# Performance work log

Hardware: AMD Instinct MI355X
Metric: run time of the kernel (lower is better)

The kernel has to match this reference:

```python
import jax, jax.numpy as jnp
import numpy as np

N_NODES = 100000
N_EDGES = 3200000
HID = 16
MP_ROUNDS = 3


def _mlp(w1, b1, w2, b2, x):
    # channels-first MLP applied per edge/node: x is [C_in, E]
    h = jax.nn.relu(w1 @ x + b1[:, None])
    return w2 @ h + b2[:, None]


def setup_inputs() -> dict:
    key = jax.random.key(0)
    ks = jax.random.split(key, 20)
    s = lambda k, shp: jax.random.normal(k, shp, dtype=jnp.float32) * 0.1
    inp = {
        "nodes": jax.random.normal(ks[0], (N_NODES,), dtype=jnp.float32),
        "edges_init": jax.random.normal(ks[1], (N_EDGES,), dtype=jnp.float32),
        "senders": jax.random.randint(ks[2], (N_EDGES,), 0, N_NODES, dtype=jnp.int32),
        "receivers": jax.random.randint(ks[3], (N_EDGES,), 0, N_NODES, dtype=jnp.int32),
        # EdgeEncoder: 1 -> HID -> HID
        "enc_w1": s(ks[4], (HID, 1)), "enc_b1": jnp.zeros((HID,), jnp.float32),
        "enc_w2": s(ks[5], (HID, HID)), "enc_b2": jnp.zeros((HID,), jnp.float32),
        # Node update MLP: (1 + 2*HID) -> HID -> 1  (shared across rounds)
        "node_w1": s(ks[6], (HID, 1 + 2 * HID)), "node_b1": jnp.zeros((HID,), jnp.float32),
        "node_w2": s(ks[7], (1, HID)), "node_b2": jnp.zeros((1,), jnp.float32),
        # Edge update MLP: (HID + 2) -> HID -> HID  (shared across rounds)
        "edge_w1": s(ks[8], (HID, HID + 2)), "edge_b1": jnp.zeros((HID,), jnp.float32),
        "edge_w2": s(ks[9], (HID, HID)), "edge_b2": jnp.zeros((HID,), jnp.float32),
        # EdgeDecoder: HID -> HID -> 1
        "dec_w1": s(ks[10], (HID, HID)), "dec_b1": jnp.zeros((HID,), jnp.float32),
        "dec_w2": s(ks[11], (1, HID)), "dec_b2": jnp.zeros((1,), jnp.float32),
        "alpha": jnp.float32(0.1),
    }
    return inp


def reference(nodes, edges_init, senders, receivers,
              enc_w1, enc_b1, enc_w2, enc_b2,
              node_w1, node_b1, node_w2, node_b2,
              edge_w1, edge_b1, edge_w2, edge_b2,
              dec_w1, dec_b1, dec_w2, dec_b2, alpha):
    n_nodes = nodes.shape[0]
    norm = jnp.abs(edges_init).max()
    e = edges_init / norm                      # [E]
    e = _mlp(enc_w1, enc_b1, enc_w2, enc_b2, e[None, :])   # [HID, E]
    for _ in range(MP_ROUNDS):                 # shared-weight MP blocks
        # gather/scatter: aggregate edge features to nodes
        agg_s = jax.ops.segment_sum(e.T, senders, num_segments=n_nodes).T     # [HID, N]
        agg_r = jax.ops.segment_sum(e.T, receivers, num_segments=n_nodes).T   # [HID, N]
        node_in = jnp.concatenate([nodes[None, :], agg_s, agg_r], axis=0)     # [1+2H, N]
        nodes = _mlp(node_w1, node_b1, node_w2, node_b2, node_in)[0]          # [N]
        edge_in = jnp.concatenate([e, nodes[senders][None, :], nodes[receivers][None, :]], axis=0)  # [H+2, E]
        e = _mlp(edge_w1, edge_b1, edge_w2, edge_b2, edge_in)                 # [HID, E]
    e = _mlp(dec_w1, dec_b1, dec_w2, dec_b2, e)[0]          # [E]
    low_tri_data = edges_init + alpha * (e * norm)          # L = L + alpha*GNN(L)
    return low_tri_data
```

## Files before the change

kernel.cpp:

```cpp
#include <hip/hip_runtime.h>
#include <hip/hip_bf16.h>

#define N_NODES 100000
#define N_EDGES 3200000
#define HID 16
#define NB 256
#define NPB 391
#define SCAP 15360
#define RCAP 15360
#define FDEPTH 32
#define LCAP1 8704
#define LCAP2 26624

static constexpr int BLK = 256;

__device__ __forceinline__ float frelu(float x) { return fmaxf(x, 0.f); }
__device__ __forceinline__ float bflo(unsigned int u) {
  return __uint_as_float(u << 16);
}
__device__ __forceinline__ float bfhi(unsigned int u) {
  return __uint_as_float(u & 0xFFFF0000u);
}
__device__ __forceinline__ unsigned int packbf(float lo, float hi) {
  __hip_bfloat16 hl = __float2bfloat16(lo), hh = __float2bfloat16(hi);
  return ((unsigned int)(*(unsigned short*)&hh) << 16) |
         (unsigned int)(*(unsigned short*)&hl);
}

union E16 {
  float4 f4[2];
  __hip_bfloat16 h[16];
};

__global__ __launch_bounds__(256) void k_norm(const float* __restrict__ edges,
                                              unsigned int* __restrict__ normbits) {
  float m = 0.f;
  for (int i = blockIdx.x * blockDim.x + threadIdx.x; i < N_EDGES;
       i += gridDim.x * blockDim.x)
    m = fmaxf(m, fabsf(edges[i]));
#pragma unroll
  for (int off = 32; off > 0; off >>= 1)
    m = fmaxf(m, __shfl_down(m, off, 64));
  __shared__ float smax[BLK / 64];
  if ((threadIdx.x & 63) == 0) smax[threadIdx.x >> 6] = m;
  __syncthreads();
  if (threadIdx.x == 0) {
    float b = smax[0];
#pragma unroll
    for (int w = 1; w < BLK / 64; ++w) b = fmaxf(b, smax[w]);
    atomicMax(normbits, __float_as_uint(b));
  }
}

__global__ __launch_bounds__(1024) void k_split(
    const int* __restrict__ senders, const int* __restrict__ receivers,
    const float* __restrict__ edges, int* __restrict__ gcnt,
    unsigned int* __restrict__ pM, float* __restrict__ pV,
    unsigned int* __restrict__ pO) {
  __shared__ __align__(16) unsigned int fM[NB][FDEPTH];
  __shared__ __align__(16) unsigned int fV[NB][FDEPTH];
  __shared__ __align__(16) unsigned int fO[NB][FDEPTH];
  __shared__ int fcnt[NB];
  const int t = threadIdx.x;
  if (t < NB) fcnt[t] = 0;
  __syncthreads();
  const int e0 = blockIdx.x * (N_EDGES / 256);
  const int e1 = e0 + (N_EDGES / 256);
  for (int base = e0; base < e1; base += 1024) {
    const int i = base + t;
    if (i < e1) {
      int s = senders[i];
      unsigned int b = (unsigned int)s / NPB;
      unsigned int m = (((unsigned int)s - b * NPB) << 22) | (unsigned int)i;
      unsigned int v = __float_as_uint(edges[i]);
      unsigned int o = (unsigned int)receivers[i];
      int pos = atomicAdd(&fcnt[b], 1);
      if (pos < FDEPTH) {
        fM[b][pos] = m; fV[b][pos] = v; fO[b][pos] = o;
      } else {
        int gb = atomicAdd(&gcnt[b], 1);
        if (gb < SCAP) {
          pM[(size_t)b * SCAP + gb] = m;
          pV[(size_t)b * SCAP + gb] = __uint_as_float(v);
          pO[(size_t)b * SCAP + gb] = o;
        }
      }
    }
    __syncthreads();
    const bool last = (base + 1024 >= e1);
    if (t < NB) {
      int c = fcnt[t]; if (c > FDEPTH) c = FDEPTH;
      int nf = last ? c : (c & ~15);
      if (nf > 0) {
        int gb = atomicAdd(&gcnt[t], nf);
        size_t db = (size_t)t * SCAP + gb;
        if ((gb & 3) == 0 && gb + nf <= SCAP) {
          int k = 0;
          for (; k + 4 <= nf; k += 4) {
            *(uint4*)(pM + db + k) = *(const uint4*)(&fM[t][k]);
            *(uint4*)((unsigned int*)pV + db + k) = *(const uint4*)(&fV[t][k]);
            *(uint4*)(pO + db + k) = *(const uint4*)(&fO[t][k]);
          }
          for (; k < nf; ++k) {
            pM[db + k] = fM[t][k]; pV[db + k] = __uint_as_float(fV[t][k]);
            pO[db + k] = fO[t][k];
          }
        } else {
          for (int k = 0; k < nf; ++k)
            if (gb + k < SCAP) {
              pM[db + k] = fM[t][k]; pV[db + k] = __uint_as_float(fV[t][k]);
              pO[db + k] = fO[t][k];
            }
        }
        int res = c - nf;
        for (int k = 0; k < res; ++k) {
          fM[t][k] = fM[t][nf + k]; fV[t][k] = fV[t][nf + k];
          fO[t][k] = fO[t][nf + k];
        }
        fcnt[t] = res;
      } else fcnt[t] = c;
    }
    __syncthreads();
  }
}

__global__ __launch_bounds__(1024) void k_bsort1(
    const unsigned int* __restrict__ pM, const float* __restrict__ pV,
    const unsigned int* __restrict__ pO, const int* __restrict__ gcnt,
    unsigned int* __restrict__ srecv, unsigned int* __restrict__ sorig,
    unsigned short* __restrict__ svalbf, unsigned int* __restrict__ ssend32,
    int* __restrict__ soff) {
  __shared__ unsigned int sM[LCAP1];
  __shared__ float sV[LCAP1];
  __shared__ unsigned int sO[LCAP1];
  __shared__ int hist[NPB], pref[NPB + 1], sc[NPB], cur[NPB];
  __shared__ int bb[NB];
  __shared__ int base_s;
  const int b = blockIdx.x, t = threadIdx.x, nt = blockDim.x;
  if (t < NB) { int c = gcnt[t]; bb[t] = c > SCAP ? SCAP : c; }
  for (int k = t; k < NPB; k += nt) hist[k] = 0;
  __syncthreads();
  if (t == 0) { int s = 0; for (int k = 0; k < b; ++k) s += bb[k]; base_s = s; }
  int nb = gcnt[b]; if (nb > SCAP) nb = SCAP;
  const unsigned int* PM = pM + (size_t)b * SCAP;
  const float* PV = pV + (size_t)b * SCAP;
  const unsigned int* PO = pO + (size_t)b * SCAP;
  for (int i = t; i < nb; i += nt) atomicAdd(&hist[PM[i] >> 22], 1);
  __syncthreads();
  if (t < NPB) sc[t] = hist[t];
  __syncthreads();
  for (int d = 1; d < NPB; d <<= 1) {
    int add = 0;
    if (t < NPB && t >= d) add = sc[t - d];
    __syncthreads();
    if (t < NPB && t >= d) sc[t] += add;
    __syncthreads();
  }
  if (t < NPB) pref[t] = sc[t] - hist[t];
  if (t == 0) pref[NPB] = sc[NPB - 1];
  __syncthreads();
  const int base = base_s;
  const int node0 = b * NPB;
  for (int k = t; k < NPB; k += nt) {
    int n = node0 + k;
    if (n < N_NODES) soff[n] = base + pref[k];
  }
  if (b == NB - 1 && t == 0) soff[N_NODES] = base + nb;
  __syncthreads();
  int klo = 0;
  while (klo < NPB) {
    int base0 = pref[klo];
    int khi = klo;
    while (khi < NPB && pref[khi + 1] - base0 <= LCAP1) ++khi;
    if (khi == klo) khi = klo + 1;
    for (int k = klo + t; k < khi; k += nt) cur[k] = pref[k];
    __syncthreads();
    for (int i = t; i < nb; i += nt) {
      unsigned int m = PM[i];
      int key = (int)(m >> 22);
      if (key >= klo && key < khi) {
        int p = atomicAdd(&cur[key], 1) - base0;
        if (p < LCAP1) { sM[p] = m; sV[p] = PV[i]; sO[p] = PO[i]; }
      }
    }
    __syncthreads();
    int csz = pref[khi] - base0;
    for (int i = t; i < csz; i += nt) {
      int g = base + base0 + i;
      unsigned int m = sM[i];
      srecv[g] = sO[i]; sorig[g] = m & 0x3FFFFFu;
      ssend32[g] = (unsigned int)(node0 + (int)(m >> 22));
      __hip_bfloat16 hb = __float2bfloat16(sV[i]);
      svalbf[g] = *(unsigned short*)&hb;
    }
    __syncthreads();
    klo = khi;
  }
}

__global__ __launch_bounds__(1024) void k_rsplit(
    const unsigned int* __restrict__ srecv, int* __restrict__ gcnt2,
    unsigned int* __restrict__ rpA) {
  __shared__ __align__(16) unsigned int fA[NB][FDEPTH];
  __shared__ int fcnt[NB];
  const int t = threadIdx.x;
  if (t < NB) fcnt[t] = 0;
  __syncthreads();
  const int e0 = blockIdx.x * (N_EDGES / 256);
  const int e1 = e0 + (N_EDGES / 256);
  for (int base = e0; base < e1; base += 1024) {
    const int i = base + t;
    if (i < e1) {
      unsigned int r = srecv[i];
      unsigned int b = r / NPB;
      unsigned int a = ((r - b * NPB) << 22) | (unsigned int)i;
      int pos = atomicAdd(&fcnt[b], 1);
      if (pos < FDEPTH) {
        fA[b][pos] = a;
      } else {
        int gb = atomicAdd(&gcnt2[b], 1);
        if (gb < RCAP) rpA[(size_t)b * RCAP + gb] = a;
      }
    }
    __syncthreads();
    const bool last = (base + 1024 >= e1);
    if (t < NB) {
      int c = fcnt[t]; if (c > FDEPTH) c = FDEPTH;
      int nf = last ? c : (c & ~15);
      if (nf > 0) {
        int gb = atomicAdd(&gcnt2[t], nf);
        size_t db = (size_t)t * RCAP + gb;
        if ((gb & 3) == 0 && gb + nf <= RCAP) {
          int k = 0;
          for (; k + 4 <= nf; k += 4)
            *(uint4*)(rpA + db + k) = *(const uint4*)(&fA[t][k]);
          for (; k < nf; ++k) rpA[db + k] = fA[t][k];
        } else {
          for (int k = 0; k < nf; ++k)
            if (gb + k < RCAP) rpA[db + k] = fA[t][k];
        }
        int res = c - nf;
        for (int k = 0; k < res; ++k) fA[t][k] = fA[t][nf + k];
        fcnt[t] = res;
      } else fcnt[t] = c;
    }
    __syncthreads();
  }
}

__global__ __launch_bounds__(1024) void k_rsort(
    const unsigned int* __restrict__ rpA, const int* __restrict__ gcnt2,
    unsigned int* __restrict__ rlist, int* __restrict__ roff) {
  __shared__ unsigned int sA[LCAP2];
  __shared__ int hist[NPB], pref[NPB + 1], sc[NPB], cur[NPB];
  __shared__ int bb[NB];
  __shared__ int base_s;
  const int b = blockIdx.x, t = threadIdx.x, nt = blockDim.x;
  if (t < NB) { int c = gcnt2[t]; bb[t] = c > RCAP ? RCAP : c; }
  for (int k = t; k < NPB; k += nt) hist[k] = 0;
  __syncthreads();
  if (t == 0) { int s = 0; for (int k = 0; k < b; ++k) s += bb[k]; base_s = s; }
  int nb = gcnt2[b]; if (nb > RCAP) nb = RCAP;
  const unsigned int* PA = rpA + (size_t)b * RCAP;
  for (int i = t; i < nb; i += nt) atomicAdd(&hist[PA[i] >> 22], 1);
  __syncthreads();
  if (t < NPB) sc[t] = hist[t];
  __syncthreads();
  for (int d = 1; d < NPB; d <<= 1) {
    int add = 0;
    if (t < NPB && t >= d) add = sc[t - d];
    __syncthreads();
    if (t < NPB && t >= d) sc[t] += add;
    __syncthreads();
  }
  if (t < NPB) pref[t] = sc[t] - hist[t];
  if (t == 0) pref[NPB] = sc[NPB - 1];
  __syncthreads();
  const int base = base_s;
  const int node0 = b * NPB;
  for (int k = t; k < NPB; k += nt) {
    int n = node0 + k;
    if (n < N_NODES) roff[n] = base + pref[k];
  }
  if (b == NB - 1 && t == 0) roff[N_NODES] = base + nb;
  __syncthreads();
  int klo = 0;
  while (klo < NPB) {
    int base0 = pref[klo];
    int khi = klo;
    while (khi < NPB && pref[khi + 1] - base0 <= LCAP2) ++khi;
    if (khi == klo) khi = klo + 1;
    for (int k = klo + t; k < khi; k += nt) cur[k] = pref[k];
    __syncthreads();
    for (int i = t; i < nb; i += nt) {
      unsigned int a = PA[i];
      int key = (int)(a >> 22);
      if (key >= klo && key < khi) {
        int p = atomicAdd(&cur[key], 1) - base0;
        if (p < LCAP2) sA[p] = a;
      }
    }
    __syncthreads();
    int csz = pref[khi] - base0;
    for (int i = t; i < csz; i += nt)
      rlist[base + base0 + i] = sA[i] & 0x3FFFFFu;
    __syncthreads();
    klo = khi;
  }
}

__global__ __launch_bounds__(256) void k_encode(
    const unsigned short* __restrict__ svalbf, const float* __restrict__ w1,
    const float* __restrict__ b1, const float* __restrict__ w2,
    const float* __restrict__ b2, const unsigned int* __restrict__ normbits,
    unsigned short* __restrict__ e) {
  int i = blockIdx.x * blockDim.x + threadIdx.x;
  float norm = __uint_as_float(*normbits);
  float x = bflo((unsigned int)svalbf[i]) / norm;
  float h[HID];
#pragma unroll
  for (int j = 0; j < HID; ++j) h[j] = frelu(fmaf(w1[j], x, b1[j]));
  E16 o;
#pragma unroll
  for (int j = 0; j < HID; ++j) {
    float acc = b2[j];
#pragma unroll
    for (int k = 0; k < HID; ++k) acc = fmaf(w2[j * HID + k], h[k], acc);
    o.h[j] = __float2bfloat16(acc);
  }
  float4* ep = (float4*)(e + (size_t)i * HID);
  ep[0] = o.f4[0];
  ep[1] = o.f4[1];
}

__global__ __launch_bounds__(256) void k_aggN(
    const unsigned short* __restrict__ e, const int* __restrict__ roff,
    const unsigned int* __restrict__ rlist, const int* __restrict__ soff,
    const float* __restrict__ nodesr, const float* __restrict__ nw1,
    const float* __restrict__ nb1_, const float* __restrict__ nw2,
    const float* __restrict__ nb2_, float* __restrict__ nodesw) {
  int wave = (blockIdx.x * blockDim.x + threadIdx.x) >> 6;
  int lane = threadIdx.x & 63, half = lane >> 5, l32 = lane & 31;
  int n = wave * 2 + half;
  int sub = l32 & 1, j16 = l32 >> 1;
  int r0 = roff[n], rdeg = roff[n + 1] - r0;
  float ar[8] = {0, 0, 0, 0, 0, 0, 0, 0};
  int q0 = 0;
  int full2 = rdeg & ~31;
  for (; q0 < full2; q0 += 32) {
    int idx0 = r0 + q0 + j16;
    unsigned int si0 = rlist[idx0];
    unsigned int si1 = rlist[idx0 + 16];
    uint4 ra = *(const uint4*)(e + (size_t)si0 * HID + sub * 8);
    uint4 rb = *(const uint4*)(e + (size_t)si1 * HID + sub * 8);
    ar[0] += bflo(ra.x); ar[1] += bfhi(ra.x);
    ar[2] += bflo(ra.y); ar[3] += bfhi(ra.y);
    ar[4] += bflo(ra.z); ar[5] += bfhi(ra.z);
    ar[6] += bflo(ra.w); ar[7] += bfhi(ra.w);
    ar[0] += bflo(rb.x); ar[1] += bfhi(rb.x);
    ar[2] += bflo(rb.y); ar[3] += bfhi(rb.y);
    ar[4] += bflo(rb.z); ar[5] += bfhi(rb.z);
    ar[6] += bflo(rb.w); ar[7] += bfhi(rb.w);
  }
  if (q0 + 16 <= rdeg) {
    int idx = r0 + q0 + j16;
    unsigned int si = rlist[idx];
    uint4 raw = *(const uint4*)(e + (size_t)si * HID + sub * 8);
    ar[0] += bflo(raw.x); ar[1] += bfhi(raw.x);
    ar[2] += bflo(raw.y); ar[3] += bfhi(raw.y);
    ar[4] += bflo(raw.z); ar[5] += bfhi(raw.z);
    ar[6] += bflo(raw.w); ar[7] += bfhi(raw.w);
    q0 += 16;
  }
  if (q0 < rdeg) {
    int slot = q0 + j16;
    bool ok = slot < rdeg;
    int idx = r0 + (ok ? slot : 0);
    unsigned int si = rlist[idx];
    uint4 raw = *(const uint4*)(e + (size_t)si * HID + sub * 8);
    float okf = ok ? 1.f : 0.f;
    ar[0] = fmaf(bflo(raw.x), okf, ar[0]); ar[1] = fmaf(bfhi(raw.x), okf, ar[1]);
    ar[2] = fmaf(bflo(raw.y), okf, ar[2]); ar[3] = fmaf(bfhi(raw.y), okf, ar[3]);
    ar[4] = fmaf(bflo(raw.z), okf, ar[4]); ar[5] = fmaf(bfhi(raw.z), okf, ar[5]);
    ar[6] = fmaf(bflo(raw.w), okf, ar[6]); ar[7] = fmaf(bfhi(raw.w), okf, ar[7]);
  }
#pragma unroll
  for (int off = 16; off >= 2; off >>= 1)
#pragma unroll
    for (int c = 0; c < 8; ++c) ar[c] += __shfl_down(ar[c], off, 64);
  int s0 = soff[n], sdeg = soff[n + 1] - s0;
  float as[16];
#pragma unroll
  for (int c = 0; c < 16; ++c) as[c] = 0.f;
  int fullB = sdeg & ~31;
  int c0 = 0;
  for (; c0 < fullB; c0 += 32) {
    int idx = s0 + c0 + l32;
    uint4 ra = *(const uint4*)(e + (size_t)idx * HID);
    uint4 rb = *(const uint4*)(e + (size_t)idx * HID + 8);
    as[0] += bflo(ra.x);  as[1] += bfhi(ra.x);
    as[2] += bflo(ra.y);  as[3] += bfhi(ra.y);
    as[4] += bflo(ra.z);  as[5] += bfhi(ra.z);
    as[6] += bflo(ra.w);  as[7] += bfhi(ra.w);
    as[8] += bflo(rb.x);  as[9] += bfhi(rb.x);
    as[10] += bflo(rb.y); as[11] += bfhi(rb.y);
    as[12] += bflo(rb.z); as[13] += bfhi(rb.z);
    as[14] += bflo(rb.w); as[15] += bfhi(rb.w);
  }
  if (c0 < sdeg) {
    int k = c0 + l32;
    bool ok = k < sdeg;
    int idx = s0 + (ok ? k : 0);
    uint4 ra = *(const uint4*)(e + (size_t)idx * HID);
    uint4 rb = *(const uint4*)(e + (size_t)idx * HID + 8);
    float okf = ok ? 1.f : 0.f;
    as[0] = fmaf(bflo(ra.x), okf, as[0]);  as[1] = fmaf(bfhi(ra.x), okf, as[1]);
    as[2] = fmaf(bflo(ra.y), okf, as[2]);  as[3] = fmaf(bfhi(ra.y), okf, as[3]);
    as[4] = fmaf(bflo(ra.z), okf, as[4]);  as[5] = fmaf(bfhi(ra.z), okf, as[5]);
    as[6] = fmaf(bflo(ra.w), okf, as[6]);  as[7] = fmaf(bfhi(ra.w), okf, as[7]);
    as[8] = fmaf(bflo(rb.x), okf, as[8]);  as[9] = fmaf(bfhi(rb.x), okf, as[9]);
    as[10] = fmaf(bflo(rb.y), okf, as[10]); as[11] = fmaf(bfhi(rb.y), okf, as[11]);
    as[12] = fmaf(bflo(rb.z), okf, as[12]); as[13] = fmaf(bfhi(rb.z), okf, as[13]);
    as[14] = fmaf(bflo(rb.w), okf, as[14]); as[15] = fmaf(bfhi(rb.w), okf, as[15]);
  }
#pragma unroll
  for (int off = 16; off >= 1; off >>= 1)
#pragma unroll
    for (int c = 0; c < 16; ++c) as[c] += __shfl_down(as[c], off, 64);
  float aS[16], aR[16];
#pragma unroll
  for (int c = 0; c < 16; ++c) aS[c] = __shfl(as[c], half * 32, 64);
#pragma unroll
  for (int k = 0; k < 8; ++k) aR[k] = __shfl(ar[k], half * 32, 64);
#pragma unroll
  for (int k = 0; k < 8; ++k) aR[8 + k] = __shfl(ar[k], half * 32 + 1, 64);
  float nsv = nodesr[n];
  float pv = 0.f;
  if (l32 < 16) {
    int j = l32;
    float a1 = fmaf(nw1[j * 33], nsv, nb1_[j]);
#pragma unroll
    for (int k = 0; k < 16; ++k) a1 = fmaf(nw1[j * 33 + 1 + k], aS[k], a1);
#pragma unroll
    for (int k = 0; k < 16; ++k) a1 = fmaf(nw1[j * 33 + 17 + k], aR[k], a1);
    pv = nw2[j] * frelu(a1);
  }
#pragma unroll
  for (int off = 8; off >= 1; off >>= 1) pv += __shfl_down(pv, off, 64);
  if (l32 == 0) nodesw[n] = pv + nb2_[0];
}

__global__ __launch_bounds__(256, 4) void k_edgeE(
    unsigned short* __restrict__ e, const unsigned int* __restrict__ srecv,
    const unsigned int* __restrict__ ssend32, const float* __restrict__ nodes,
    const float* __restrict__ w1, const float* __restrict__ b1,
    const float* __restrict__ w2, const float* __restrict__ b2) {
  int i0 = (blockIdx.x * blockDim.x + threadIdx.x) * 2;
  float ns[2], nr[2];
#pragma unroll
  for (int q = 0; q < 2; ++q) {
    ns[q] = nodes[ssend32[i0 + q]];
    nr[q] = nodes[srecv[i0 + q]];
  }
  unsigned int pk[2][8];
#pragma unroll
  for (int q = 0; q < 2; ++q) {
    const uint4* ep = (const uint4*)(e + (size_t)(i0 + q) * HID);
    uint4 ra = ep[0], rb = ep[1];
    pk[q][0] = ra.x; pk[q][1] = ra.y; pk[q][2] = ra.z; pk[q][3] = ra.w;
    pk[q][4] = rb.x; pk[q][5] = rb.y; pk[q][6] = rb.z; pk[q][7] = rb.w;
  }
  float h[2][16];
#pragma unroll
  for (int j = 0; j < 16; ++j) {
    float wA = w1[j * 18 + 16], wB = w1[j * 18 + 17], bb = b1[j];
#pragma unroll
    for (int q = 0; q < 2; ++q)
      h[q][j] = fmaf(wA, ns[q], fmaf(wB, nr[q], bb));
  }
#pragma unroll
  for (int kp = 0; kp < 8; ++kp) {
    float x0[2], x1[2];
#pragma unroll
    for (int q = 0; q < 2; ++q) {
      x0[q] = bflo(pk[q][kp]);
      x1[q] = bfhi(pk[q][kp]);
    }
#pragma unroll
    for (int j = 0; j < 16; ++j) {
      float wA = w1[j * 18 + 2 * kp], wB = w1[j * 18 + 2 * kp + 1];
#pragma unroll
      for (int q = 0; q < 2; ++q)
        h[q][j] = fmaf(wB, x1[q], fmaf(wA, x0[q], h[q][j]));
    }
  }
#pragma unroll
  for (int j = 0; j < 16; ++j)
#pragma unroll
    for (int q = 0; q < 2; ++q) h[q][j] = frelu(h[q][j]);
#pragma unroll
  for (int c0 = 0; c0 < 16; c0 += 8) {
    float y[2][8];
#pragma unroll
    for (int cc = 0; cc < 8; ++cc) {
      float bv = b2[c0 + cc];
#pragma unroll
      for (int q = 0; q < 2; ++q) y[q][cc] = bv;
    }
#pragma unroll
    for (int j = 0; j < 16; ++j) {
#pragma unroll
      for (int cc = 0; cc < 8; ++cc) {
        float wv = w2[(c0 + cc) * HID + j];
#pragma unroll
        for (int q = 0; q < 2; ++q) y[q][cc] = fmaf(wv, h[q][j], y[q][cc]);
      }
    }
#pragma unroll
    for (int q = 0; q < 2; ++q) {
      uint4 o = make_uint4(packbf(y[q][0], y[q][1]), packbf(y[q][2], y[q][3]),
                           packbf(y[q][4], y[q][5]), packbf(y[q][6], y[q][7]));
      *(uint4*)(e + (size_t)(i0 + q) * HID + c0) = o;
    }
  }
}

__global__ __launch_bounds__(256, 4) void k_final(
    const unsigned short* __restrict__ e, const unsigned int* __restrict__ srecv,
    const unsigned int* __restrict__ ssend32, const unsigned int* __restrict__ sorig,
    const float* __restrict__ nodes, const float* __restrict__ ew1,
    const float* __restrict__ eb1, const float* __restrict__ ew2,
    const float* __restrict__ eb2, const float* __restrict__ dw1,
    const float* __restrict__ db1, const float* __restrict__ dw2,
    const float* __restrict__ db2, const unsigned int* __restrict__ normbits,
    const float* __restrict__ alpha, float* __restrict__ out) {
  int i0 = (blockIdx.x * blockDim.x + threadIdx.x) * 2;
  float ns[2], nr[2];
#pragma unroll
  for (int q = 0; q < 2; ++q) {
    ns[q] = nodes[ssend32[i0 + q]];
    nr[q] = nodes[srecv[i0 + q]];
  }
  unsigned int pk[2][8];
#pragma unroll
  for (int q = 0; q < 2; ++q) {
    const uint4* ep = (const uint4*)(e + (size_t)(i0 + q) * HID);
    uint4 ra = ep[0], rb = ep[1];
    pk[q][0] = ra.x; pk[q][1] = ra.y; pk[q][2] = ra.z; pk[q][3] = ra.w;
    pk[q][4] = rb.x; pk[q][5] = rb.y; pk[q][6] = rb.z; pk[q][7] = rb.w;
  }
  float h[2][16];
#pragma unroll
  for (int j = 0; j < 16; ++j) {
    float wA = ew1[j * 18 + 16], wB = ew1[j * 18 + 17], bb = eb1[j];
#pragma unroll
    for (int q = 0; q < 2; ++q)
      h[q][j] = fmaf(wA, ns[q], fmaf(wB, nr[q], bb));
  }
#pragma unroll
  for (int kp = 0; kp < 8; ++kp) {
    float x0[2], x1[2];
#pragma unroll
    for (int q = 0; q < 2; ++q) {
      x0[q] = bflo(pk[q][kp]);
      x1[q] = bfhi(pk[q][kp]);
    }
#pragma unroll
    for (int j = 0; j < 16; ++j) {
      float wA = ew1[j * 18 + 2 * kp], wB = ew1[j * 18 + 2 * kp + 1];
#pragma unroll
      for (int q = 0; q < 2; ++q)
        h[q][j] = fmaf(wB, x1[q], fmaf(wA, x0[q], h[q][j]));
    }
  }
#pragma unroll
  for (int j = 0; j < 16; ++j)
#pragma unroll
    for (int q = 0; q < 2; ++q) h[q][j] = frelu(h[q][j]);
  float y[2][16];
#pragma unroll
  for (int c = 0; c < 16; ++c) {
    float bv = eb2[c];
#pragma unroll
    for (int q = 0; q < 2; ++q) y[q][c] = bv;
  }
#pragma unroll
  for (int j = 0; j < 16; ++j) {
#pragma unroll
    for (int c = 0; c < 16; ++c) {
      float wv = ew2[c * HID + j];
#pragma unroll
      for (int q = 0; q < 2; ++q) y[q][c] = fmaf(wv, h[q][j], y[q][c]);
    }
  }
  float d[2] = {db2[0], db2[0]};
#pragma unroll
  for (int j = 0; j < 16; ++j) {
    float a1[2] = {db1[j], db1[j]};
#pragma unroll
    for (int k = 0; k < 16; ++k) {
      float wv = dw1[j * HID + k];
#pragma unroll
      for (int q = 0; q < 2; ++q) a1[q] = fmaf(wv, y[q][k], a1[q]);
    }
    float wd = dw2[j];
#pragma unroll
    for (int q = 0; q < 2; ++q) d[q] = fmaf(wd, frelu(a1[q]), d[q]);
  }
  float alphaN = alpha[0] * __uint_as_float(*normbits);
#pragma unroll
  for (int q = 0; q < 2; ++q) out[sorig[i0 + q]] = alphaN * d[q];
}

__global__ __launch_bounds__(256) void k_resid(const float* __restrict__ edges,
                                               float* __restrict__ out) {
  int i = blockIdx.x * blockDim.x + threadIdx.x;
  out[i] += edges[i];
}

extern "C" void kernel_launch(void* const* d_in, const int* in_sizes, int n_in,
                              void* d_out, int out_size, void* d_ws,
                              size_t ws_size, hipStream_t stream) {
  const float* nodes0 = (const float*)d_in[0];
  const float* edges0 = (const float*)d_in[1];
  const int* senders = (const int*)d_in[2];
  const int* receivers = (const int*)d_in[3];
  const float* enc_w1 = (const float*)d_in[4];
  const float* enc_b1 = (const float*)d_in[5];
  const float* enc_w2 = (const float*)d_in[6];
  const float* enc_b2 = (const float*)d_in[7];
  const float* node_w1 = (const float*)d_in[8];
  const float* node_b1 = (const float*)d_in[9];
  const float* node_w2 = (const float*)d_in[10];
  const float* node_b2 = (const float*)d_in[11];
  const float* edge_w1 = (const float*)d_in[12];
  const float* edge_b1 = (const float*)d_in[13];
  const float* edge_w2 = (const float*)d_in[14];
  const float* edge_b2 = (const float*)d_in[15];
  const float* dec_w1 = (const float*)d_in[16];
  const float* dec_b1 = (const float*)d_in[17];
  const float* dec_w2 = (const float*)d_in[18];
  const float* dec_b2 = (const float*)d_in[19];
  const float* alpha = (const float*)d_in[20];

  char* ws = (char*)d_ws;
  unsigned short* e = (unsigned short*)ws;
  char* p = ws + (size_t)N_EDGES * HID * 2;
  unsigned int* srecv = (unsigned int*)p;    p += (size_t)N_EDGES * 4;
  unsigned int* sorig = (unsigned int*)p;    p += (size_t)N_EDGES * 4;
  unsigned int* rlist = (unsigned int*)p;    p += (size_t)N_EDGES * 4;
  unsigned int* ssend32 = (unsigned int*)p;  p += (size_t)N_EDGES * 4;
  unsigned short* svalbf = (unsigned short*)p; p += (size_t)N_EDGES * 2;
  int* soff = (int*)p;                       p += (size_t)(N_NODES + 16) * 4;
  int* roff = (int*)p;                       p += (size_t)(N_NODES + 16) * 4;
  float* nbA = (float*)p;                    p += (size_t)N_NODES * 4;
  float* nbB = (float*)p;                    p += (size_t)N_NODES * 4;
  unsigned int* normbits = (unsigned int*)p; p += 64;
  int* gcnt = (int*)p;                       p += NB * 4;
  int* gcnt2 = (int*)p;                      p += NB * 4;
  unsigned int* pM = (unsigned int*)ws;
  float* pV = (float*)(ws + (size_t)NB * SCAP * 4);
  unsigned int* pO = (unsigned int*)(ws + (size_t)NB * SCAP * 8);
  unsigned int* rpA = (unsigned int*)(ws + (size_t)NB * SCAP * 12);

  const int ngrid = 12500;
  const int egrid = N_EDGES / BLK;
  const int egrid2 = N_EDGES / (BLK * 2);

  hipMemsetAsync(normbits, 0, 64 + 2 * NB * 4, stream);
  k_norm<<<512, BLK, 0, stream>>>(edges0, normbits);
  k_split<<<256, 1024, 0, stream>>>(senders, receivers, edges0, gcnt, pM, pV, pO);
  k_bsort1<<<NB, 1024, 0, stream>>>(pM, pV, pO, gcnt, srecv, sorig, svalbf,
                                    ssend32, soff);
  k_rsplit<<<256, 1024, 0, stream>>>(srecv, gcnt2, rpA);
  k_rsort<<<NB, 1024, 0, stream>>>(rpA, gcnt2, rlist, roff);
  k_encode<<<egrid, BLK, 0, stream>>>(svalbf, enc_w1, enc_b1, enc_w2, enc_b2,
                                      normbits, e);
  k_aggN<<<ngrid, BLK, 0, stream>>>(e, roff, rlist, soff, nodes0, node_w1,
                                    node_b1, node_w2, node_b2, nbA);
  k_edgeE<<<egrid2, BLK, 0, stream>>>(e, srecv, ssend32, nbA, edge_w1,
                                      edge_b1, edge_w2, edge_b2);
  k_aggN<<<ngrid, BLK, 0, stream>>>(e, roff, rlist, soff, nbA, node_w1,
                                    node_b1, node_w2, node_b2, nbB);
  k_edgeE<<<egrid2, BLK, 0, stream>>>(e, srecv, ssend32, nbB, edge_w1,
                                      edge_b1, edge_w2, edge_b2);
  k_aggN<<<ngrid, BLK, 0, stream>>>(e, roff, rlist, soff, nbB, node_w1,
                                    node_b1, node_w2, node_b2, nbA);
  k_final<<<egrid2, BLK, 0, stream>>>(e, srecv, ssend32, sorig, nbA, edge_w1,
                                      edge_b1, edge_w2, edge_b2, dec_w1,
                                      dec_b1, dec_w2, dec_b2, normbits, alpha,
                                      (float*)d_out);
  k_resid<<<egrid, BLK, 0, stream>>>(edges0, (float*)d_out);
}
```

Baseline: 846.7 us.

## Compute per-edge MLPs with bf16 MFMA 16x16x32 instead of scalar FMAs

Rewrites the edge-update and final edge+decoder kernels so that each wave processes 64 edges in four tiles of 16 using bf16 MFMA instructions. Weights are loaded once as A fragments and edge features as B fragments, with node values packed into the K padding. Intermediate activations are redistributed between layers with lane shuffles. This moves the compute-bound FMA work onto matrix cores, at the cost of bf16 rounding of the weights, node values and hidden activations, extra shuffle traffic, and a changed memory access pattern.

Measured after the change: 905.9 us. +7.0%, slower.

```diff
diff --git a/kernel.cpp b/kernel.cpp
--- a/kernel.cpp
+++ b/kernel.cpp
@@ -14,6 +14,9 @@
 
 static constexpr int BLK = 256;
 
+typedef __attribute__((ext_vector_type(8))) short bf16x8;
+typedef __attribute__((ext_vector_type(4))) float f32x4;
+
 __device__ __forceinline__ float frelu(float x) { return fmaxf(x, 0.f); }
 __device__ __forceinline__ float bflo(unsigned int u) {
   return __uint_as_float(u << 16);
@@ -25,6 +28,10 @@
   __hip_bfloat16 hl = __float2bfloat16(lo), hh = __float2bfloat16(hi);
   return ((unsigned int)(*(unsigned short*)&hh) << 16) |
          (unsigned int)(*(unsigned short*)&hl);
+}
+__device__ __forceinline__ short f2bs(float v) {
+  __hip_bfloat16 hb = __float2bfloat16(v);
+  return *(short*)&hb;
 }
 
 union E16 {
@@ -450,82 +457,63 @@
   if (l32 == 0) nodesw[n] = pv + nb2_[0];
 }
 
-__global__ __launch_bounds__(256, 4) void k_edgeE(
+__global__ __launch_bounds__(256) void k_edgeM(
     unsigned short* __restrict__ e, const unsigned int* __restrict__ srecv,
     const unsigned int* __restrict__ ssend32, const float* __restrict__ nodes,
     const float* __restrict__ w1, const float* __restrict__ b1,
     const float* __restrict__ w2, const float* __restrict__ b2) {
-  int i0 = (blockIdx.x * blockDim.x + threadIdx.x) * 2;
-  float ns[2], nr[2];
-#pragma unroll
-  for (int q = 0; q < 2; ++q) {
-    ns[q] = nodes[ssend32[i0 + q]];
-    nr[q] = nodes[srecv[i0 + q]];
-  }
-  unsigned int pk[2][8];
-#pragma unroll
-  for (int q = 0; q < 2; ++q) {
-    const uint4* ep = (const uint4*)(e + (size_t)(i0 + q) * HID);
-    uint4 ra = ep[0], rb = ep[1];
-    pk[q][0] = ra.x; pk[q][1] = ra.y; pk[q][2] = ra.z; pk[q][3] = ra.w;
-    pk[q][4] = rb.x; pk[q][5] = rb.y; pk[q][6] = rb.z; pk[q][7] = rb.w;
-  }
-  float h[2][16];
-#pragma unroll
-  for (int j = 0; j < 16; ++j) {
-    float wA = w1[j * 18 + 16], wB = w1[j * 18 + 17], bb = b1[j];
-#pragma unroll
-    for (int q = 0; q < 2; ++q)
-      h[q][j] = fmaf(wA, ns[q], fmaf(wB, nr[q], bb));
-  }
-#pragma unroll
-  for (int kp = 0; kp < 8; ++kp) {
-    float x0[2], x1[2];
-#pragma unroll
-    for (int q = 0; q < 2; ++q) {
-      x0[q] = bflo(pk[q][kp]);
-      x1[q] = bfhi(pk[q][kp]);
-    }
-#pragma unroll
-    for (int j = 0; j < 16; ++j) {
-      float wA = w1[j * 18 + 2 * kp], wB = w1[j * 18 + 2 * kp + 1];
-#pragma unroll
-      for (int q = 0; q < 2; ++q)
-        h[q][j] = fmaf(wB, x1[q], fmaf(wA, x0[q], h[q][j]));
-    }
-  }
-#pragma unroll
-  for (int j = 0; j < 16; ++j)
-#pragma unroll
-    for (int q = 0; q < 2; ++q) h[q][j] = frelu(h[q][j]);
-#pragma unroll
-  for (int c0 = 0; c0 < 16; c0 += 8) {
-    float y[2][8];
-#pragma unroll
-    for (int cc = 0; cc < 8; ++cc) {
-      float bv = b2[c0 + cc];
-#pragma unroll
-      for (int q = 0; q < 2; ++q) y[q][cc] = bv;
-    }
-#pragma unroll
-    for (int j = 0; j < 16; ++j) {
-#pragma unroll
-      for (int cc = 0; cc < 8; ++cc) {
-        float wv = w2[(c0 + cc) * HID + j];
-#pragma unroll
-        for (int q = 0; q < 2; ++q) y[q][cc] = fmaf(wv, h[q][j], y[q][cc]);
+  int wave = (blockIdx.x * blockDim.x + threadIdx.x) >> 6;
+  int l = threadIdx.x & 63;
+  int c = l & 15, kg = l >> 4;
+  bf16x8 a1, a2;
+#pragma unroll
+  for (int j = 0; j < 8; ++j) {
+    int k = kg * 8 + j;
+    a1[j] = f2bs(k < 18 ? w1[c * 18 + k] : 0.f);
+    a2[j] = f2bs(k < 16 ? w2[c * 16 + k] : 0.f);
+  }
+  f32x4 c1, c2;
+#pragma unroll
+  for (int j = 0; j < 4; ++j) {
+    c1[j] = b1[4 * kg + j];
+    c2[j] = b2[4 * kg + j];
+  }
+  int T0 = wave * 64;
+#pragma unroll
+  for (int t = 0; t < 4; ++t) {
+    int T = T0 + t * 16;
+    int ec = T + c;
+    bf16x8 bfrag = {};
+    if (kg < 2) {
+      uint4 raw = *(const uint4*)(e + (size_t)ec * HID + kg * 8);
+      bfrag = *(bf16x8*)&raw;
+    } else if (kg == 2) {
+      bfrag[0] = f2bs(nodes[ssend32[ec]]);
+      bfrag[1] = f2bs(nodes[srecv[ec]]);
+    }
+    f32x4 d1 = __builtin_amdgcn_mfma_f32_16x16x32_bf16(a1, bfrag, c1, 0, 0, 0);
+#pragma unroll
+    for (int j = 0; j < 4; ++j) d1[j] = fmaxf(d1[j], 0.f);
+    bf16x8 b2f = {};
+    int src0 = ((2 * kg) * 16 + c) & 63;
+    int src1 = ((2 * kg + 1) * 16 + c) & 63;
+#pragma unroll
+    for (int j = 0; j < 4; ++j) {
+      float v = __shfl(d1[j], src0, 64);
+      float w = __shfl(d1[j], src1, 64);
+      if (kg < 2) {
+        b2f[j] = f2bs(v);
+        b2f[4 + j] = f2bs(w);
       }
     }
-#pragma unroll
-    for (int q = 0; q < 2; ++q) {
-      uint4 o = make_uint4(packbf(y[q][0], y[q][1]), packbf(y[q][2], y[q][3]),
-                           packbf(y[q][4], y[q][5]), packbf(y[q][6], y[q][7]));
-      *(uint4*)(e + (size_t)(i0 + q) * HID + c0) = o;
-    }
-  }
-}
-
-__global__ __launch_bounds__(256, 4) void k_final(
+    f32x4 d2 = __builtin_amdgcn_mfma_f32_16x16x32_bf16(a2, b2f, c2, 0, 0, 0);
+    unsigned int u0 = packbf(d2[0], d2[1]);
+    unsigned int u1 = packbf(d2[2], d2[3]);
+    *(uint2*)(e + (size_t)ec * HID + 4 * kg) = make_uint2(u0, u1);
+  }
+}
+
+__global__ __launch_bounds__(256) void k_final(
     const unsigned short* __restrict__ e, const unsigned int* __restrict__ srecv,
     const unsigned int* __restrict__ ssend32, const unsigned int* __restrict__ sorig,
     const float* __restrict__ nodes, const float* __restrict__ ew1,
@@ -534,82 +522,76 @@
     const float* __restrict__ db1, const float* __restrict__ dw2,
     const float* __restrict__ db2, const unsigned int* __restrict__ normbits,
     const float* __restrict__ alpha, float* __restrict__ out) {
-  int i0 = (blockIdx.x * blockDim.x + threadIdx.x) * 2;
-  float ns[2], nr[2];
-#pragma unroll
-  for (int q = 0; q < 2; ++q) {
-    ns[q] = nodes[ssend32[i0 + q]];
-    nr[q] = nodes[srecv[i0 + q]];
-  }
-  unsigned int pk[2][8];
-#pragma unroll
-  for (int q = 0; q < 2; ++q) {
-    const uint4* ep = (const uint4*)(e + (size_t)(i0 + q) * HID);
-    uint4 ra = ep[0], rb = ep[1];
-    pk[q][0] = ra.x; pk[q][1] = ra.y; pk[q][2] = ra.z; pk[q][3] = ra.w;
-    pk[q][4] = rb.x; pk[q][5] = rb.y; pk[q][6] = rb.z; pk[q][7] = rb.w;
-  }
-  float h[2][16];
-#pragma unroll
-  for (int j = 0; j < 16; ++j) {
-    float wA = ew1[j * 18 + 16], wB = ew1[j * 18 + 17], bb = eb1[j];
-#pragma unroll
-    for (int q = 0; q < 2; ++q)
-      h[q][j] = fmaf(wA, ns[q], fmaf(wB, nr[q], bb));
-  }
-#pragma unroll
-  for (int kp = 0; kp < 8; ++kp) {
-    float x0[2], x1[2];
-#pragma unroll
-    for (int q = 0; q < 2; ++q) {
-      x0[q] = bflo(pk[q][kp]);
-      x1[q] = bfhi(pk[q][kp]);
-    }
-#pragma unroll
-    for (int j = 0; j < 16; ++j) {
-      float wA = ew1[j * 18 + 2 * kp], wB = ew1[j * 18 + 2 * kp + 1];
-#pragma unroll
-      for (int q = 0; q < 2; ++q)
-        h[q][j] = fmaf(wB, x1[q], fmaf(wA, x0[q], h[q][j]));
-    }
-  }
-#pragma unroll
-  for (int j = 0; j < 16; ++j)
-#pragma unroll
-    for (int q = 0; q < 2; ++q) h[q][j] = frelu(h[q][j]);
-  float y[2][16];
-#pragma unroll
-  for (int c = 0; c < 16; ++c) {
-    float bv = eb2[c];
-#pragma unroll
-    for (int q = 0; q < 2; ++q) y[q][c] = bv;
-  }
-#pragma unroll
-  for (int j = 0; j < 16; ++j) {
-#pragma unroll
-    for (int c = 0; c < 16; ++c) {
-      float wv = ew2[c * HID + j];
-#pragma unroll
-      for (int q = 0; q < 2; ++q) y[q][c] = fmaf(wv, h[q][j], y[q][c]);
-    }
-  }
-  float d[2] = {db2[0], db2[0]};
-#pragma unroll
-  for (int j = 0; j < 16; ++j) {
-    float a1[2] = {db1[j], db1[j]};
-#pragma unroll
-    for (int k = 0; k < 16; ++k) {
-      float wv = dw1[j * HID + k];
-#pragma unroll
-      for (int q = 0; q < 2; ++q) a1[q] = fmaf(wv, y[q][k], a1[q]);
-    }
-    float wd = dw2[j];
-#pragma unroll
-    for (int q = 0; q < 2; ++q) d[q] = fmaf(wd, frelu(a1[q]), d[q]);
+  int wave = (blockIdx.x * blockDim.x + threadIdx.x) >> 6;
+  int l = threadIdx.x & 63;
+  int c = l & 15, kg = l >> 6 ? 0 : (l >> 4);
+  kg = l >> 4;
+  bf16x8 a1, a2, a3;
+#pragma unroll
+  for (int j = 0; j < 8; ++j) {
+    int k = kg * 8 + j;
+    a1[j] = f2bs(k < 18 ? ew1[c * 18 + k] : 0.f);
+    a2[j] = f2bs(k < 16 ? ew2[c * 16 + k] : 0.f);
+    a3[j] = f2bs(k < 16 ? dw1[c * 16 + k] : 0.f);
+  }
+  f32x4 c1, c2, c3;
+  float w2v[4];
+#pragma unroll
+  for (int j = 0; j < 4; ++j) {
+    c1[j] = eb1[4 * kg + j];
+    c2[j] = eb2[4 * kg + j];
+    c3[j] = db1[4 * kg + j];
+    w2v[j] = dw2[4 * kg + j];
   }
   float alphaN = alpha[0] * __uint_as_float(*normbits);
-#pragma unroll
-  for (int q = 0; q < 2; ++q) out[sorig[i0 + q]] = alphaN * d[q];
+  float db2v = db2[0];
+  int T0 = wave * 64;
+#pragma unroll
+  for (int t = 0; t < 4; ++t) {
+    int T = T0 + t * 16;
+    int ec = T + c;
+    bf16x8 bfrag = {};
+    if (kg < 2) {
+      uint4 raw = *(const uint4*)(e + (size_t)ec * HID + kg * 8);
+      bfrag = *(bf16x8*)&raw;
+    } else if (kg == 2) {
+      bfrag[0] = f2bs(nodes[ssend32[ec]]);
+      bfrag[1] = f2bs(nodes[srecv[ec]]);
+    }
+    f32x4 d1 = __builtin_amdgcn_mfma_f32_16x16x32_bf16(a1, bfrag, c1, 0, 0, 0);
+#pragma unroll
+    for (int j = 0; j < 4; ++j) d1[j] = fmaxf(d1[j], 0.f);
+    int src0 = ((2 * kg) * 16 + c) & 63;
+    int src1 = ((2 * kg + 1) * 16 + c) & 63;
+    bf16x8 b2f = {};
+#pragma unroll
+    for (int j = 0; j < 4; ++j) {
+      float v = __shfl(d1[j], src0, 64);
+      float w = __shfl(d1[j], src1, 64);
+      if (kg < 2) {
+        b2f[j] = f2bs(v);
+        b2f[4 + j] = f2bs(w);
+      }
+    }
+    f32x4 d2 = __builtin_amdgcn_mfma_f32_16x16x32_bf16(a2, b2f, c2, 0, 0, 0);
+    bf16x8 b3f = {};
+#pragma unroll
+    for (int j = 0; j < 4; ++j) {
+      float v = __shfl(d2[j], src0, 64);
+      float w = __shfl(d2[j], src1, 64);
+      if (kg < 2) {
+        b3f[j] = f2bs(v);
+        b3f[4 + j] = f2bs(w);
+      }
+    }
+    f32x4 d3 = __builtin_amdgcn_mfma_f32_16x16x32_bf16(a3, b3f, c3, 0, 0, 0);
+    float p = 0.f;
+#pragma unroll
+    for (int j = 0; j < 4; ++j) p = fmaf(w2v[j], fmaxf(d3[j], 0.f), p);
+    p += __shfl_down(p, 32, 64);
+    p += __shfl_down(p, 16, 64);
+    if (kg == 0) out[sorig[ec]] = alphaN * (p + db2v);
+  }
 }
 
 __global__ __launch_bounds__(256) void k_resid(const float* __restrict__ edges,
@@ -665,7 +647,7 @@
 
   const int ngrid = 12500;
   const int egrid = N_EDGES / BLK;
-  const int egrid2 = N_EDGES / (BLK * 2);
+  const int mgrid = N_EDGES / 256;
 
   hipMemsetAsync(normbits, 0, 64 + 2 * NB * 4, stream);
   k_norm<<<512, BLK, 0, stream>>>(edges0, normbits);
@@ -678,17 +660,17 @@
                                       normbits, e);
   k_aggN<<<ngrid, BLK, 0, stream>>>(e, roff, rlist, soff, nodes0, node_w1,
                                     node_b1, node_w2, node_b2, nbA);
-  k_edgeE<<<egrid2, BLK, 0, stream>>>(e, srecv, ssend32, nbA, edge_w1,
-                                      edge_b1, edge_w2, edge_b2);
+  k_edgeM<<<mgrid, BLK, 0, stream>>>(e, srecv, ssend32, nbA, edge_w1,
+                                     edge_b1, edge_w2, edge_b2);
   k_aggN<<<ngrid, BLK, 0, stream>>>(e, roff, rlist, soff, nbA, node_w1,
                                     node_b1, node_w2, node_b2, nbB);
-  k_edgeE<<<egrid2, BLK, 0, stream>>>(e, srecv, ssend32, nbB, edge_w1,
-                                      edge_b1, edge_w2, edge_b2);
+  k_edgeM<<<mgrid, BLK, 0, stream>>>(e, srecv, ssend32, nbB, edge_w1,
+                                     edge_b1, edge_w2, edge_b2);
   k_aggN<<<ngrid, BLK, 0, stream>>>(e, roff, rlist, soff, nbB, node_w1,
                                     node_b1, node_w2, node_b2, nbA);
-  k_final<<<egrid2, BLK, 0, stream>>>(e, srecv, ssend32, sorig, nbA, edge_w1,
-                                      edge_b1, edge_w2, edge_b2, dec_w1,
-                                      dec_b1, dec_w2, dec_b2, normbits, alpha,
-                                      (float*)d_out);
+  k_final<<<mgrid, BLK, 0, stream>>>(e, srecv, ssend32, sorig, nbA, edge_w1,
+                                     edge_b1, edge_w2, edge_b2, dec_w1, dec_b1,
+                                     dec_w2, dec_b2, normbits, alpha,
+                                     (float*)d_out);
   k_resid<<<egrid, BLK, 0, stream>>>(edges0, (float*)d_out);
 }
```
